# Kernel tuning notes

Hardware: AMD Instinct MI355X
Metric: run time of the kernel (lower is better)

The kernel has to match this reference:

```python
import jax, jax.numpy as jnp
import numpy as np
from jax import lax

H = 106      # hidden size
IN = 100     # input feature size
S = 512      # sequence length (time-major)
B = 256      # batch
N_REST = 10  # layers 2..6 of lstm1 (5) + all 5 layers of lstm2, all 106->106


def _lstm_layer(x, Wih, Whh, bih, bhh):
    """Single LSTM layer, PyTorch gate order (i, f, g, o). x: (S, B, in)."""
    # Precompute input contribution for all timesteps at once: (S, B, 4H)
    gx = jnp.einsum('sbi,gi->sbg', x, Wih) + bih + bhh

    def step(carry, g_t):
        h, c = carry
        g = g_t + h @ Whh.T                      # (B, 4H)
        i, f, gg, o = jnp.split(g, 4, axis=-1)
        i = jax.nn.sigmoid(i)
        f = jax.nn.sigmoid(f)
        gg = jnp.tanh(gg)
        o = jax.nn.sigmoid(o)
        c = f * c + i * gg
        h = o * jnp.tanh(c)
        return (h, c), h

    b = x.shape[1]
    h0 = jnp.zeros((b, H), x.dtype)
    c0 = jnp.zeros((b, H), x.dtype)
    _, ys = lax.scan(step, (h0, c0), gx)
    return ys  # (S, B, H)


def setup_inputs() -> dict:
    key = jax.random.key(0)
    ks = jax.random.split(key, 10)
    k = 1.0 / np.sqrt(H)  # PyTorch LSTM default uniform init bound
    u = lambda kk, shape: jax.random.uniform(kk, shape, jnp.float32, -k, k)

    noise = jax.random.normal(ks[0], (S, B, IN), jnp.float32)
    # First layer: input dim 100
    W_ih0 = u(ks[1], (4 * H, IN))
    W_hh0 = u(ks[2], (4 * H, H))
    b_ih0 = u(ks[3], (4 * H,))
    b_hh0 = u(ks[4], (4 * H,))
    # Remaining 10 layers: input dim 106, stacked
    W_ih = u(ks[5], (N_REST, 4 * H, H))
    W_hh = u(ks[6], (N_REST, 4 * H, H))
    b_ih = u(ks[7], (N_REST, 4 * H))
    b_hh = u(ks[8], (N_REST, 4 * H))
    return {"noise": noise, "W_ih0": W_ih0, "W_hh0": W_hh0, "b_ih0": b_ih0,
            "b_hh0": b_hh0, "W_ih": W_ih, "W_hh": W_hh, "b_ih": b_ih, "b_hh": b_hh}


def reference(noise, W_ih0, W_hh0, b_ih0, b_hh0, W_ih, W_hh, b_ih, b_hh):
    x = _lstm_layer(noise, W_ih0, W_hh0, b_ih0, b_hh0)

    def layer_step(xc, params):
        Wih, Whh, bih, bhh = params
        return _lstm_layer(xc, Wih, Whh, bih, bhh), None

    x, _ = lax.scan(layer_step, x, (W_ih, W_hh, b_ih, b_hh))
    return x  # (S, B, H)
```

## Files before the change

kernel.cpp:

```cpp
#include <hip/hip_runtime.h>
#include <cmath>


namespace {
constexpr int H = 106, G4 = 424, SEQ = 512, BB = 256, KIN0 = 100;
constexpr int UST = 392;
constexpr int GST = 436;
constexpr int NTHR = 896;
constexpr int RGN = 16;
constexpr int NLAYER = 11;
constexpr int RD = 16;
constexpr int REL = 56;
constexpr size_t CNT_STRIDE = 16;
constexpr size_t RING_OFF_B = 65536;
constexpr size_t RING_PER_L = (size_t)RD * BB * REL;

using f16x8 = __attribute__((ext_vector_type(8))) _Float16;
using f32x4 = __attribute__((ext_vector_type(4))) float;
typedef unsigned long long u64;

__device__ __forceinline__ u64 ald(const u64* p) {
    return __hip_atomic_load(p, __ATOMIC_RELAXED, __HIP_MEMORY_SCOPE_AGENT);
}
__device__ __forceinline__ void ast(u64* p, u64 v) {
    __hip_atomic_store(p, v, __ATOMIC_RELAXED, __HIP_MEMORY_SCOPE_AGENT);
}
__device__ __forceinline__ void spinc(const unsigned* p, unsigned tgt) {
    while (__hip_atomic_load(p, __ATOMIC_RELAXED, __HIP_MEMORY_SCOPE_AGENT) < tgt)
        __builtin_amdgcn_s_sleep(8);
}
__device__ __forceinline__ float fast_tanh(float x) {
    float t = __expf(2.0f * x);
    return 1.0f - 2.0f / (t + 1.0f);
}
__device__ __forceinline__ float act_gate(float g, bool istanh) {
    float s = istanh ? 2.0f * g : g;
    float r = 1.0f / (1.0f + __expf(-s));
    return istanh ? 2.0f * r - 1.0f : r;
}
__device__ __forceinline__ unsigned packh2(float a, float b) {
    unsigned lo = (unsigned)__builtin_bit_cast(unsigned short, (_Float16)a);
    unsigned hi = (unsigned)__builtin_bit_cast(unsigned short, (_Float16)b);
    return (hi << 16) | lo;
}

__global__ __launch_bounds__(NTHR)
__attribute__((amdgpu_waves_per_eu(4, 4)))
void lstm_wave(const float* __restrict__ noise,
               float* __restrict__ yout,
               unsigned* cnt, u64* ring,
               const float* __restrict__ W_ih0, const float* __restrict__ W_hh0,
               const float* __restrict__ b_ih0, const float* __restrict__ b_hh0,
               const float* __restrict__ W_ih,  const float* __restrict__ W_hh,
               const float* __restrict__ b_ih,  const float* __restrict__ b_hh)
{
    const int l = blockIdx.x / RGN;
    const int rg = blockIdx.x % RGN;
    const bool LAST = (l == NLAYER - 1);
    const int K_IN = (l == 0) ? KIN0 : H;

    const float* Wih = (l == 0) ? W_ih0 : W_ih + (size_t)(l - 1) * G4 * H;
    const float* Whh = (l == 0) ? W_hh0 : W_hh + (size_t)(l - 1) * G4 * H;
    const float* pbi = (l == 0) ? b_ih0 : b_ih + (size_t)(l - 1) * G4;
    const float* pbh = (l == 0) ? b_hh0 : b_hh + (size_t)(l - 1) * G4;

    unsigned* cons_my = cnt + (size_t)(l * RGN + rg) * CNT_STRIDE;
    unsigned* cons_in = cnt + (size_t)((l - 1) * RGN + rg) * CNT_STRIDE;
    u64* ring_in  = ring + (size_t)(l - 1) * RING_PER_L;
    u64* ring_out = ring + (size_t)l * RING_PER_L;

    __shared__ __align__(16) _Float16 su[16 * UST];
    __shared__ float gl[16 * GST];

    const int tid = threadIdx.x;
    const int w = tid >> 6, lane = tid & 63;
    const int l16 = lane & 15, kg = lane >> 4;
    const int lm = tid / 56, ld = tid % 56;

    f16x8 bf[2][8];
    float bias[2];
    #pragma unroll
    for (int t = 0; t < 2; ++t) {
        const int n = 16 * (2 * w + t) + l16;
        const bool valid = n < G4;
        const float* pwx = Wih + (size_t)(valid ? n : 0) * K_IN;
        const float* pwh = Whh + (size_t)(valid ? n : 0) * H;
        #pragma unroll
        for (int q = 0; q < 8; ++q) {
            f16x8 v;
            #pragma unroll
            for (int e = 0; e < 8; ++e) {
                const int k = 32 * q + 8 * kg + e;
                float f = 0.0f;
                if (valid) {
                    if (k < 128) { if (k < K_IN) f = pwx[k]; }
                    else { const int kh = k - 128; if (kh < H) f = pwh[kh]; }
                }
                v[e] = (_Float16)f;
            }
            bf[t][q] = v;
        }
        bias[t] = valid ? (pbi[n] + pbh[n]) : 0.0f;
    }

    for (int i = tid; i < 16 * (UST / 2); i += NTHR) ((unsigned*)su)[i] = 0;
    float c0 = 0.0f, c1 = 0.0f;
    __syncthreads();
    {
        unsigned xr = 0;
        if (l == 0) {
            if (ld < 50) {
                const float2 v = *(const float2*)(noise + ((size_t)rg * 16 + lm) * KIN0 + 2 * ld);
                xr = packh2(v.x, v.y);
            }
        } else {
            const u64* p = ring_in + ((size_t)0 * BB + rg * 16 + lm) * REL + ld;
            u64 v = ald(p);
            while ((unsigned)(v >> 32) != 1u) { __builtin_amdgcn_s_sleep(1); v = ald(p); }
            xr = (unsigned)v;
        }
        ((unsigned*)su)[lm * 196 + ld] = xr;
    }
    __syncthreads();

    const int um = tid / 53, up = tid % 53;

    for (int s = 0; s < SEQ; ++s) {
        u64 v = 0; unsigned xr = 0;
        const bool wantx = (s + 1 < SEQ);
        const u64* pin = ring_in + ((size_t)((s + 1) % RD) * BB + rg * 16 + lm) * REL + ld;
        if (wantx) {
            if (l == 0) {
                if (ld < 50) {
                    const float2 t = *(const float2*)(noise + ((size_t)(s + 1) * BB + rg * 16 + lm) * KIN0 + 2 * ld);
                    xr = packh2(t.x, t.y);
                }
            } else {
                v = ald(pin);
            }
        }
        if (tid == 0 && !LAST && s >= RD && (s & 7) == 0)
            spinc(cons_my, (unsigned)(s - 8));

        const _Float16* arow = su + (size_t)l16 * UST;
        const _Float16* ax = arow + (s & 1) * 128 + 8 * kg;
        f32x4 acc[2] = {{0, 0, 0, 0}, {0, 0, 0, 0}};
        #pragma unroll
        for (int q = 0; q < 4; ++q) {
            const f16x8 a = *(const f16x8*)(ax + 32 * q);
            acc[0] = __builtin_amdgcn_mfma_f32_16x16x32_f16(a, bf[0][q], acc[0], 0, 0, 0);
            acc[1] = __builtin_amdgcn_mfma_f32_16x16x32_f16(a, bf[1][q], acc[1], 0, 0, 0);
        }
        const _Float16* ah = arow + 256 + 8 * kg;
        #pragma unroll
        for (int q = 4; q < 8; ++q) {
            const f16x8 a = *(const f16x8*)(ah + 32 * (q - 4));
            acc[0] = __builtin_amdgcn_mfma_f32_16x16x32_f16(a, bf[0][q], acc[0], 0, 0, 0);
            acc[1] = __builtin_amdgcn_mfma_f32_16x16x32_f16(a, bf[1][q], acc[1], 0, 0, 0);
        }
        #pragma unroll
        for (int t = 0; t < 2; ++t) {
            const int n = 16 * (2 * w + t) + l16;
            if (n < G4) {
                const bool istanh = (n >= 2 * H) && (n < 3 * H);
                #pragma unroll
                for (int r = 0; r < 4; ++r)
                    gl[(4 * kg + r) * GST + n] = act_gate(acc[t][r] + bias[t], istanh);
            }
        }
        if (wantx) {
            if (l > 0) {
                const unsigned expt = (unsigned)(s + 2);
                while ((unsigned)(v >> 32) != expt) { __builtin_amdgcn_s_sleep(1); v = ald(pin); }
                xr = (unsigned)v;
            }
            ((unsigned*)su)[lm * 196 + ((s + 1) & 1) * 64 + ld] = xr;
        }
        __syncthreads();

        if (tid < 848) {
            const float* gm = gl + um * GST;
            const float2 vi = *(const float2*)(gm + 2 * up);
            const float2 vf = *(const float2*)(gm + H + 2 * up);
            const float2 vg = *(const float2*)(gm + 2 * H + 2 * up);
            const float2 vo = *(const float2*)(gm + 3 * H + 2 * up);
            c0 = fmaf(vf.x, c0, vi.x * vg.x);
            c1 = fmaf(vf.y, c1, vi.y * vg.y);
            const float h0 = vo.x * fast_tanh(c0);
            const float h1 = vo.y * fast_tanh(c1);
            const unsigned hw = packh2(h0, h1);
            ((unsigned*)su)[um * 196 + 128 + up] = hw;
            if (LAST) {
                *(float2*)(yout + ((size_t)s * BB + rg * 16 + um) * H + 2 * up) =
                    make_float2(h0, h1);
            } else {
                ast(ring_out + ((size_t)(s % RD) * BB + rg * 16 + um) * REL + up,
                    ((u64)(unsigned)(s + 1) << 32) | hw);
            }
        } else if (!LAST) {
            const int t2 = tid - 848, m = t2 / 3, dd = t2 % 3;
            ast(ring_out + ((size_t)(s % RD) * BB + rg * 16 + m) * REL + 53 + dd,
                (u64)(unsigned)(s + 1) << 32);
        }
        __syncthreads();

        if (tid == 0 && l > 0 && s + 1 < SEQ)
            __hip_atomic_store(cons_in, (unsigned)(s + 2),
                               __ATOMIC_RELAXED, __HIP_MEMORY_SCOPE_AGENT);
    }
}
}

extern "C" void kernel_launch(void* const* d_in, const int* in_sizes, int n_in,
                              void* d_out, int out_size, void* d_ws, size_t ws_size,
                              hipStream_t stream) {
    const float* noise = (const float*)d_in[0];
    const float* W_ih0 = (const float*)d_in[1];
    const float* W_hh0 = (const float*)d_in[2];
    const float* b_ih0 = (const float*)d_in[3];
    const float* b_hh0 = (const float*)d_in[4];
    const float* W_ih  = (const float*)d_in[5];
    const float* W_hh  = (const float*)d_in[6];
    const float* b_ih  = (const float*)d_in[7];
    const float* b_hh  = (const float*)d_in[8];

    const size_t clear_bytes = RING_OFF_B + (size_t)NLAYER * RING_PER_L * sizeof(u64);
    hipMemsetAsync(d_ws, 0, clear_bytes, stream);

    unsigned* cnt = (unsigned*)d_ws;
    u64* ring = (u64*)((char*)d_ws + RING_OFF_B);

    lstm_wave<<<dim3(NLAYER * RGN), dim3(NTHR), 0, stream>>>(
        noise, (float*)d_out, cnt, ring,
        W_ih0, W_hh0, b_ih0, b_hh0, W_ih, W_hh, b_ih, b_hh);
}
```

Measured before the change: 1.419 ms.

## Precompute next-step input MFMA and prefetch ring input two steps ahead

The input-projection half of the per-step MFMA (x part) is moved out of the critical recurrent path: it is computed for step s+1 in the phase after the cell update, overlapping with the ring stores, so each step only performs the h-dependent MFMAs before activations. The ring-buffer load for the upstream layer's output is also issued two steps ahead (vnext/vprev) to hide global latency. This adds accumulator registers and relies on the x buffer for s+1 already being written before the second barrier.

```diff
diff --git a/kernel.cpp b/kernel.cpp
--- a/kernel.cpp
+++ b/kernel.cpp
@@ -124,33 +124,35 @@
     __syncthreads();
 
     const int um = tid / 53, up = tid % 53;
+    const _Float16* arow = su + (size_t)l16 * UST;
+
+    f32x4 accx[2] = {{0, 0, 0, 0}, {0, 0, 0, 0}};
+    {
+        const _Float16* ax = arow + 8 * kg;
+        #pragma unroll
+        for (int q = 0; q < 4; ++q) {
+            const f16x8 a = *(const f16x8*)(ax + 32 * q);
+            accx[0] = __builtin_amdgcn_mfma_f32_16x16x32_f16(a, bf[0][q], accx[0], 0, 0, 0);
+            accx[1] = __builtin_amdgcn_mfma_f32_16x16x32_f16(a, bf[1][q], accx[1], 0, 0, 0);
+        }
+    }
+    u64 vprev = 0;
+    if (l > 0) vprev = ald(ring_in + ((size_t)(1 % RD) * BB + rg * 16 + lm) * REL + ld);
 
     for (int s = 0; s < SEQ; ++s) {
-        u64 v = 0; unsigned xr = 0;
+        u64 vnext = 0; unsigned xr = 0;
         const bool wantx = (s + 1 < SEQ);
-        const u64* pin = ring_in + ((size_t)((s + 1) % RD) * BB + rg * 16 + lm) * REL + ld;
-        if (wantx) {
-            if (l == 0) {
-                if (ld < 50) {
-                    const float2 t = *(const float2*)(noise + ((size_t)(s + 1) * BB + rg * 16 + lm) * KIN0 + 2 * ld);
-                    xr = packh2(t.x, t.y);
-                }
-            } else {
-                v = ald(pin);
-            }
+        if (l > 0) {
+            if (s + 2 < SEQ)
+                vnext = ald(ring_in + ((size_t)((s + 2) % RD) * BB + rg * 16 + lm) * REL + ld);
+        } else if (wantx && ld < 50) {
+            const float2 t = *(const float2*)(noise + ((size_t)(s + 1) * BB + rg * 16 + lm) * KIN0 + 2 * ld);
+            xr = packh2(t.x, t.y);
         }
         if (tid == 0 && !LAST && s >= RD && (s & 7) == 0)
             spinc(cons_my, (unsigned)(s - 8));
 
-        const _Float16* arow = su + (size_t)l16 * UST;
-        const _Float16* ax = arow + (s & 1) * 128 + 8 * kg;
-        f32x4 acc[2] = {{0, 0, 0, 0}, {0, 0, 0, 0}};
-        #pragma unroll
-        for (int q = 0; q < 4; ++q) {
-            const f16x8 a = *(const f16x8*)(ax + 32 * q);
-            acc[0] = __builtin_amdgcn_mfma_f32_16x16x32_f16(a, bf[0][q], acc[0], 0, 0, 0);
-            acc[1] = __builtin_amdgcn_mfma_f32_16x16x32_f16(a, bf[1][q], acc[1], 0, 0, 0);
-        }
+        f32x4 acc[2] = {accx[0], accx[1]};
         const _Float16* ah = arow + 256 + 8 * kg;
         #pragma unroll
         for (int q = 4; q < 8; ++q) {
@@ -171,11 +173,13 @@
         if (wantx) {
             if (l > 0) {
                 const unsigned expt = (unsigned)(s + 2);
-                while ((unsigned)(v >> 32) != expt) { __builtin_amdgcn_s_sleep(1); v = ald(pin); }
-                xr = (unsigned)v;
+                const u64* pin = ring_in + ((size_t)((s + 1) % RD) * BB + rg * 16 + lm) * REL + ld;
+                while ((unsigned)(vprev >> 32) != expt) { __builtin_amdgcn_s_sleep(1); vprev = ald(pin); }
+                xr = (unsigned)vprev;
             }
             ((unsigned*)su)[lm * 196 + ((s + 1) & 1) * 64 + ld] = xr;
         }
+        vprev = vnext;
         __syncthreads();
 
         if (tid < 848) {
@@ -202,6 +206,17 @@
             ast(ring_out + ((size_t)(s % RD) * BB + rg * 16 + m) * REL + 53 + dd,
                 (u64)(unsigned)(s + 1) << 32);
         }
+        if (wantx) {
+            const _Float16* ax = arow + ((s + 1) & 1) * 128 + 8 * kg;
+            accx[0] = f32x4{0, 0, 0, 0};
+            accx[1] = f32x4{0, 0, 0, 0};
+            #pragma unroll
+            for (int q = 0; q < 4; ++q) {
+                const f16x8 a = *(const f16x8*)(ax + 32 * q);
+                accx[0] = __builtin_amdgcn_mfma_f32_16x16x32_f16(a, bf[0][q], accx[0], 0, 0, 0);
+                accx[1] = __builtin_amdgcn_mfma_f32_16x16x32_f16(a, bf[1][q], accx[1], 0, 0, 0);
+            }
+        }
         __syncthreads();
 
         if (tid == 0 && l > 0 && s + 1 < SEQ)
```

Result: faster. 1.352 ms (-4.7%).

## Batch input ring reads in chunks of eight timesteps per wavefront pipeline

Applied to the files above, without the earlier changes.

Each layer block now fetches and waits for eight timesteps of input from the upstream ring at once, staging them in a multi-slot shared buffer, instead of polling one timestep ahead. Consumer-progress signalling moves to once per chunk. The aim is to amortise global-memory polling latency and one barrier per step across the chunk. In exchange, pipeline latency between layers grows by up to eight steps, which lengthens the fill of the 11-layer wavefront. The memset is also trimmed to skip the last layer's unused ring.

```diff
diff --git a/kernel.cpp b/kernel.cpp
--- a/kernel.cpp
+++ b/kernel.cpp
@@ -4,13 +4,13 @@
 
 namespace {
 constexpr int H = 106, G4 = 424, SEQ = 512, BB = 256, KIN0 = 100;
-constexpr int UST = 392;
 constexpr int GST = 436;
 constexpr int NTHR = 896;
 constexpr int RGN = 16;
 constexpr int NLAYER = 11;
 constexpr int RD = 16;
 constexpr int REL = 56;
+constexpr int KMAC = 8;
 constexpr size_t CNT_STRIDE = 16;
 constexpr size_t RING_OFF_B = 65536;
 constexpr size_t RING_PER_L = (size_t)RD * BB * REL;
@@ -25,9 +25,14 @@
 __device__ __forceinline__ void ast(u64* p, u64 v) {
     __hip_atomic_store(p, v, __ATOMIC_RELAXED, __HIP_MEMORY_SCOPE_AGENT);
 }
+__device__ __forceinline__ unsigned aldu(const unsigned* p) {
+    return __hip_atomic_load(p, __ATOMIC_RELAXED, __HIP_MEMORY_SCOPE_AGENT);
+}
+__device__ __forceinline__ void astu(unsigned* p, unsigned v) {
+    __hip_atomic_store(p, v, __ATOMIC_RELAXED, __HIP_MEMORY_SCOPE_AGENT);
+}
 __device__ __forceinline__ void spinc(const unsigned* p, unsigned tgt) {
-    while (__hip_atomic_load(p, __ATOMIC_RELAXED, __HIP_MEMORY_SCOPE_AGENT) < tgt)
-        __builtin_amdgcn_s_sleep(8);
+    while (aldu(p) < tgt) __builtin_amdgcn_s_sleep(8);
 }
 __device__ __forceinline__ float fast_tanh(float x) {
     float t = __expf(2.0f * x);
@@ -69,13 +74,15 @@
     u64* ring_in  = ring + (size_t)(l - 1) * RING_PER_L;
     u64* ring_out = ring + (size_t)l * RING_PER_L;
 
-    __shared__ __align__(16) _Float16 su[16 * UST];
+    __shared__ __align__(16) _Float16 sx[KMAC][16 * 136];
+    __shared__ __align__(16) _Float16 sh[16 * 136];
     __shared__ float gl[16 * GST];
 
     const int tid = threadIdx.x;
     const int w = tid >> 6, lane = tid & 63;
     const int l16 = lane & 15, kg = lane >> 4;
     const int lm = tid / 56, ld = tid % 56;
+    const int um = tid / 53, up = tid % 53;
 
     f16x8 bf[2][8];
     float bias[2];
@@ -103,110 +110,106 @@
         bias[t] = valid ? (pbi[n] + pbh[n]) : 0.0f;
     }
 
-    for (int i = tid; i < 16 * (UST / 2); i += NTHR) ((unsigned*)su)[i] = 0;
+    for (int i = tid; i < KMAC * 1088 + 1088; i += NTHR) {
+        if (i < KMAC * 1088) ((unsigned*)sx)[i] = 0;
+        else ((unsigned*)sh)[i - KMAC * 1088] = 0;
+    }
     float c0 = 0.0f, c1 = 0.0f;
     __syncthreads();
-    {
-        unsigned xr = 0;
+
+    for (int m = 0; m < SEQ / KMAC; ++m) {
+        unsigned xw[KMAC] = {0, 0, 0, 0, 0, 0, 0, 0};
         if (l == 0) {
             if (ld < 50) {
-                const float2 v = *(const float2*)(noise + ((size_t)rg * 16 + lm) * KIN0 + 2 * ld);
-                xr = packh2(v.x, v.y);
+                #pragma unroll
+                for (int ss = 0; ss < KMAC; ++ss) {
+                    const int s = KMAC * m + ss;
+                    const float2 t = *(const float2*)(noise +
+                        ((size_t)s * BB + rg * 16 + lm) * KIN0 + 2 * ld);
+                    xw[ss] = packh2(t.x, t.y);
+                }
             }
         } else {
-            const u64* p = ring_in + ((size_t)0 * BB + rg * 16 + lm) * REL + ld;
-            u64 v = ald(p);
-            while ((unsigned)(v >> 32) != 1u) { __builtin_amdgcn_s_sleep(1); v = ald(p); }
-            xr = (unsigned)v;
-        }
-        ((unsigned*)su)[lm * 196 + ld] = xr;
-    }
-    __syncthreads();
-
-    const int um = tid / 53, up = tid % 53;
-
-    for (int s = 0; s < SEQ; ++s) {
-        u64 v = 0; unsigned xr = 0;
-        const bool wantx = (s + 1 < SEQ);
-        const u64* pin = ring_in + ((size_t)((s + 1) % RD) * BB + rg * 16 + lm) * REL + ld;
-        if (wantx) {
-            if (l == 0) {
-                if (ld < 50) {
-                    const float2 t = *(const float2*)(noise + ((size_t)(s + 1) * BB + rg * 16 + lm) * KIN0 + 2 * ld);
-                    xr = packh2(t.x, t.y);
-                }
-            } else {
-                v = ald(pin);
-            }
-        }
-        if (tid == 0 && !LAST && s >= RD && (s & 7) == 0)
-            spinc(cons_my, (unsigned)(s - 8));
-
-        const _Float16* arow = su + (size_t)l16 * UST;
-        const _Float16* ax = arow + (s & 1) * 128 + 8 * kg;
-        f32x4 acc[2] = {{0, 0, 0, 0}, {0, 0, 0, 0}};
-        #pragma unroll
-        for (int q = 0; q < 4; ++q) {
-            const f16x8 a = *(const f16x8*)(ax + 32 * q);
-            acc[0] = __builtin_amdgcn_mfma_f32_16x16x32_f16(a, bf[0][q], acc[0], 0, 0, 0);
-            acc[1] = __builtin_amdgcn_mfma_f32_16x16x32_f16(a, bf[1][q], acc[1], 0, 0, 0);
-        }
-        const _Float16* ah = arow + 256 + 8 * kg;
-        #pragma unroll
-        for (int q = 4; q < 8; ++q) {
-            const f16x8 a = *(const f16x8*)(ah + 32 * (q - 4));
-            acc[0] = __builtin_amdgcn_mfma_f32_16x16x32_f16(a, bf[0][q], acc[0], 0, 0, 0);
-            acc[1] = __builtin_amdgcn_mfma_f32_16x16x32_f16(a, bf[1][q], acc[1], 0, 0, 0);
-        }
-        #pragma unroll
-        for (int t = 0; t < 2; ++t) {
-            const int n = 16 * (2 * w + t) + l16;
-            if (n < G4) {
-                const bool istanh = (n >= 2 * H) && (n < 3 * H);
-                #pragma unroll
-                for (int r = 0; r < 4; ++r)
-                    gl[(4 * kg + r) * GST + n] = act_gate(acc[t][r] + bias[t], istanh);
-            }
-        }
-        if (wantx) {
-            if (l > 0) {
-                const unsigned expt = (unsigned)(s + 2);
-                while ((unsigned)(v >> 32) != expt) { __builtin_amdgcn_s_sleep(1); v = ald(pin); }
-                xr = (unsigned)v;
-            }
-            ((unsigned*)su)[lm * 196 + ((s + 1) & 1) * 64 + ld] = xr;
+            u64 v[KMAC];
+            #pragma unroll
+            for (int ss = 0; ss < KMAC; ++ss) {
+                const int s = KMAC * m + ss;
+                v[ss] = ald(ring_in + ((size_t)(s & (RD - 1)) * BB + rg * 16 + lm) * REL + ld);
+            }
+            #pragma unroll
+            for (int ss = 0; ss < KMAC; ++ss) {
+                const int s = KMAC * m + ss;
+                const unsigned expt = (unsigned)(s + 1);
+                const u64* pin = ring_in + ((size_t)(s & (RD - 1)) * BB + rg * 16 + lm) * REL + ld;
+                u64 vv = v[ss];
+                while ((unsigned)(vv >> 32) != expt) { __builtin_amdgcn_s_sleep(2); vv = ald(pin); }
+                xw[ss] = (unsigned)vv;
+            }
+        }
+        if (tid == 0 && !LAST && m >= 2) spinc(cons_my, (unsigned)(KMAC * m - 8));
+        if (l > 0 || ld < 50) {
+            #pragma unroll
+            for (int ss = 0; ss < KMAC; ++ss)
+                ((unsigned*)sx)[ss * 1088 + lm * 68 + ld] = xw[ss];
         }
         __syncthreads();
-
-        if (tid < 848) {
-            const float* gm = gl + um * GST;
-            const float2 vi = *(const float2*)(gm + 2 * up);
-            const float2 vf = *(const float2*)(gm + H + 2 * up);
-            const float2 vg = *(const float2*)(gm + 2 * H + 2 * up);
-            const float2 vo = *(const float2*)(gm + 3 * H + 2 * up);
-            c0 = fmaf(vf.x, c0, vi.x * vg.x);
-            c1 = fmaf(vf.y, c1, vi.y * vg.y);
-            const float h0 = vo.x * fast_tanh(c0);
-            const float h1 = vo.y * fast_tanh(c1);
-            const unsigned hw = packh2(h0, h1);
-            ((unsigned*)su)[um * 196 + 128 + up] = hw;
-            if (LAST) {
-                *(float2*)(yout + ((size_t)s * BB + rg * 16 + um) * H + 2 * up) =
-                    make_float2(h0, h1);
-            } else {
-                ast(ring_out + ((size_t)(s % RD) * BB + rg * 16 + um) * REL + up,
-                    ((u64)(unsigned)(s + 1) << 32) | hw);
-            }
-        } else if (!LAST) {
-            const int t2 = tid - 848, m = t2 / 3, dd = t2 % 3;
-            ast(ring_out + ((size_t)(s % RD) * BB + rg * 16 + m) * REL + 53 + dd,
-                (u64)(unsigned)(s + 1) << 32);
-        }
-        __syncthreads();
-
-        if (tid == 0 && l > 0 && s + 1 < SEQ)
-            __hip_atomic_store(cons_in, (unsigned)(s + 2),
-                               __ATOMIC_RELAXED, __HIP_MEMORY_SCOPE_AGENT);
+        if (tid == 0 && l > 0) astu(cons_in, (unsigned)(KMAC * m + KMAC));
+
+        for (int ss = 0; ss < KMAC; ++ss) {
+            const int s = KMAC * m + ss;
+            f32x4 acc[2] = {{0, 0, 0, 0}, {0, 0, 0, 0}};
+            const _Float16* ax = &sx[ss][l16 * 136 + 8 * kg];
+            #pragma unroll
+            for (int q = 0; q < 4; ++q) {
+                const f16x8 a = *(const f16x8*)(ax + 32 * q);
+                acc[0] = __builtin_amdgcn_mfma_f32_16x16x32_f16(a, bf[0][q], acc[0], 0, 0, 0);
+                acc[1] = __builtin_amdgcn_mfma_f32_16x16x32_f16(a, bf[1][q], acc[1], 0, 0, 0);
+            }
+            const _Float16* ah = &sh[l16 * 136 + 8 * kg];
+            #pragma unroll
+            for (int q = 4; q < 8; ++q) {
+                const f16x8 a = *(const f16x8*)(ah + 32 * (q - 4));
+                acc[0] = __builtin_amdgcn_mfma_f32_16x16x32_f16(a, bf[0][q], acc[0], 0, 0, 0);
+                acc[1] = __builtin_amdgcn_mfma_f32_16x16x32_f16(a, bf[1][q], acc[1], 0, 0, 0);
+            }
+            #pragma unroll
+            for (int t = 0; t < 2; ++t) {
+                const int n = 16 * (2 * w + t) + l16;
+                if (n < G4) {
+                    const bool istanh = (n >= 2 * H) && (n < 3 * H);
+                    #pragma unroll
+                    for (int r = 0; r < 4; ++r)
+                        gl[(4 * kg + r) * GST + n] = act_gate(acc[t][r] + bias[t], istanh);
+                }
+            }
+            __syncthreads();
+
+            if (tid < 848) {
+                const float* gm = gl + um * GST;
+                const float2 vi = *(const float2*)(gm + 2 * up);
+                const float2 vf = *(const float2*)(gm + H + 2 * up);
+                const float2 vg = *(const float2*)(gm + 2 * H + 2 * up);
+                const float2 vo = *(const float2*)(gm + 3 * H + 2 * up);
+                c0 = fmaf(vf.x, c0, vi.x * vg.x);
+                c1 = fmaf(vf.y, c1, vi.y * vg.y);
+                const float h0 = vo.x * fast_tanh(c0);
+                const float h1 = vo.y * fast_tanh(c1);
+                const unsigned hw = packh2(h0, h1);
+                ((unsigned*)sh)[um * 68 + up] = hw;
+                if (LAST) {
+                    *(float2*)(yout + ((size_t)s * BB + rg * 16 + um) * H + 2 * up) =
+                        make_float2(h0, h1);
+                } else {
+                    ast(ring_out + ((size_t)(s & (RD - 1)) * BB + rg * 16 + um) * REL + up,
+                        ((u64)(unsigned)(s + 1) << 32) | hw);
+                }
+            } else if (!LAST) {
+                const int t2 = tid - 848, mm = t2 / 3, dd = t2 % 3;
+                ast(ring_out + ((size_t)(s & (RD - 1)) * BB + rg * 16 + mm) * REL + 53 + dd,
+                    (u64)(unsigned)(s + 1) << 32);
+            }
+            __syncthreads();
+        }
     }
 }
 }
@@ -224,7 +227,7 @@
     const float* b_ih  = (const float*)d_in[7];
     const float* b_hh  = (const float*)d_in[8];
 
-    const size_t clear_bytes = RING_OFF_B + (size_t)NLAYER * RING_PER_L * sizeof(u64);
+    const size_t clear_bytes = RING_OFF_B + (size_t)10 * RING_PER_L * sizeof(u64);
     hipMemsetAsync(d_ws, 0, clear_bytes, stream);
 
     unsigned* cnt = (unsigned*)d_ws;
```

After: 1.287 ms. 1.1x faster.
